# Kernel optimization log

Measured on AMD Instinct MI355X. Metric: run time of the kernel, lower is better.

## Reference

```python
import jax, jax.numpy as jnp
import numpy as np
from math import sqrt

B, T, C = 2, 2048, 2048
H = 16
NOPE, ROPE, VD, LORA = 128, 64, 128, 512
QK = NOPE + ROPE  # 192
EPS = 1e-6


def _make_freq_cis(T, rope_dim):
    inv = 1.0 / (10000.0 ** (np.arange(0, rope_dim, 2, dtype=np.float32) / rope_dim))
    t = np.arange(T, dtype=np.float32)
    ang = np.outer(t, inv)  # [T, rope_dim/2]
    return jnp.asarray(np.stack([np.cos(ang), np.sin(ang)], -1))  # [T, rope_dim/2, 2]


def setup_inputs() -> dict:
    key = jax.random.key(0)
    ks = jax.random.split(key, 6)
    x = jax.random.normal(ks[0], (B, T, C), jnp.float32)
    freq_cis = _make_freq_cis(T, ROPE)
    causal = jnp.where(jnp.tril(jnp.ones((T, T), bool)), 0.0, -1e9).astype(jnp.float32)
    Wq = jax.random.normal(ks[1], (C, H * QK), jnp.float32) * (1.0 / sqrt(C))
    Wckv = jax.random.normal(ks[2], (C, LORA + ROPE), jnp.float32) * (1.0 / sqrt(C))
    kv_norm_w = jnp.ones((LORA,), jnp.float32)
    Wdkv = jax.random.normal(ks[3], (LORA, H * (NOPE + VD)), jnp.float32) * (1.0 / sqrt(LORA))
    Wproj = jax.random.normal(ks[4], (H * VD, C), jnp.float32) * (1.0 / sqrt(H * VD))
    return {"x": x, "freq_cis": freq_cis, "mask": causal, "window": causal,
            "Wq": Wq, "Wckv": Wckv, "kv_norm_w": kv_norm_w, "Wdkv": Wdkv,
            "Wproj": Wproj, "start_pos": 0}


def apply_rope(x, freq_cis):
    # x: [B, T, h, D]; freq_cis: [T, D/2, 2]
    b, t, h, d = x.shape
    xr = x.reshape(b, t, h, d // 2, 2)
    fc = freq_cis.reshape(1, t, 1, d // 2, 2)
    real = xr[..., 0] * fc[..., 0] - xr[..., 1] * fc[..., 1]
    imag = xr[..., 1] * fc[..., 0] + xr[..., 0] * fc[..., 1]
    return jnp.stack([real, imag], -1).reshape(b, t, h, d)


def rms_norm(x, w, eps=EPS):
    return x * jax.lax.rsqrt(jnp.mean(x * x, -1, keepdims=True) + eps) * w


def reference(x, freq_cis, mask, window, Wq, Wckv, kv_norm_w, Wdkv, Wproj, start_pos):
    del window, start_pos  # Global attention, no KV cache (prefill)
    b, t, _ = x.shape
    q = (x @ Wq).reshape(b, t, H, QK)
    q_nope, q_rope = q[..., :NOPE], q[..., NOPE:]
    q_rope = apply_rope(q_rope, freq_cis)

    ckv = x @ Wckv  # [B, T, LORA+ROPE]
    kv_lat, k_rope = ckv[..., :LORA], ckv[..., LORA:]
    k_rope = apply_rope(k_rope.reshape(b, t, 1, ROPE), freq_cis)  # [B,T,1,ROPE]

    kv = rms_norm(kv_lat, kv_norm_w) @ Wdkv  # [B, T, H*(NOPE+VD)]
    kv = kv.reshape(b, t, H, NOPE + VD)
    k_nope, v = kv[..., :NOPE], kv[..., NOPE:]

    q = jnp.concatenate([q_nope, q_rope], -1)                                   # [B,T,H,QK]
    k = jnp.concatenate([k_nope, jnp.broadcast_to(k_rope, (b, t, H, ROPE))], -1)

    scale = 1.0 / sqrt(QK)
    atten = jnp.einsum('bqhd,bkhd->bhqk', q, k) * scale + mask  # [B,H,T,T]
    atten = jax.nn.softmax(atten, -1)
    out = jnp.einsum('bhqk,bkhd->bqhd', atten, v).reshape(b, t, H * VD)
    return out @ Wproj
```

## Files before the change

kernel.cpp:

```cpp
#include <hip/hip_runtime.h>
#include <hip/hip_bf16.h>
#include <math.h>


typedef short bf16x8 __attribute__((ext_vector_type(8)));
typedef short short4v __attribute__((ext_vector_type(4)));
typedef float f32x4 __attribute__((ext_vector_type(4)));
typedef float f32x16 __attribute__((ext_vector_type(16)));

#define MFMA16(a, b, c) __builtin_amdgcn_mfma_f32_16x16x32_bf16(a, b, c, 0, 0, 0)
#define MFMA32(a, b, c) __builtin_amdgcn_mfma_f32_32x32x16_bf16(a, b, c, 0, 0, 0)

__device__ __forceinline__ short f2bf(float f) {
  union { float f; unsigned u; } v; v.f = f;
  unsigned r = v.u + 0x7fffu + ((v.u >> 16) & 1u);
  return (short)(r >> 16);
}
__device__ __forceinline__ float bf2f(short s) {
  union { unsigned u; float f; } v;
  v.u = ((unsigned)(unsigned short)s) << 16;
  return v.f;
}
__device__ __forceinline__ unsigned cvtpk(float a, float b) {
  unsigned r;
  asm("v_cvt_pk_bf16_f32 %0, %1, %2" : "=v"(r) : "v"(a), "v"(b));
  return r;
}
__device__ __forceinline__ void gl16(const void* g, void* l) {
  __builtin_amdgcn_global_load_lds(
      (const __attribute__((address_space(1))) unsigned int*)g,
      (__attribute__((address_space(3))) unsigned int*)l, 16, 0, 0);
}
#define CFENCE() asm volatile("" ::: "memory")
#define HWBAR()  do { CFENCE(); __builtin_amdgcn_s_barrier(); CFENCE(); } while (0)

__global__ __launch_bounds__(256) void cvt_k(const float* __restrict__ in,
                                             short* __restrict__ out, int n) {
  int i = (blockIdx.x * 256 + threadIdx.x) * 8;
  if (i >= n) return;
  float4 a = *(const float4*)(in + i);
  float4 b = *(const float4*)(in + i + 4);
  bf16x8 o;
  o[0] = f2bf(a.x); o[1] = f2bf(a.y); o[2] = f2bf(a.z); o[3] = f2bf(a.w);
  o[4] = f2bf(b.x); o[5] = f2bf(b.y); o[6] = f2bf(b.z); o[7] = f2bf(b.w);
  *(bf16x8*)(out + i) = o;
}

__global__ __launch_bounds__(256) void tcvt_k(const float* __restrict__ W,
                                              short* __restrict__ out,
                                              int K, int N, int Np, int row_off) {
  __shared__ float tile[32][33];
  int k0 = blockIdx.x * 32, n0 = blockIdx.y * 32;
  int tx = threadIdx.x & 31, ty = threadIdx.x >> 5;
#pragma unroll
  for (int j = 0; j < 4; j++) {
    int k = k0 + ty + j * 8, n = n0 + tx;
    tile[ty + j * 8][tx] = (n < N) ? W[(size_t)k * N + n] : 0.f;
  }
  __syncthreads();
#pragma unroll
  for (int j = 0; j < 4; j++) {
    int n = n0 + ty + j * 8;
    out[(size_t)(row_off + n) * K + k0 + tx] = f2bf(tile[tx][ty + j * 8]);
  }
}

template <int MODE, int BM, int BN, int SGL>
__global__ __launch_bounds__(512, 2) void gemm8_k(const short* __restrict__ A,
                                                  const short* __restrict__ Bt,
                                                  void* __restrict__ C1,
                                                  void* __restrict__ C2,
                                                  int M, int N, int K, int nbx) {
  constexpr int FM = BM / 32;
  constexpr int FN = BN / 64;
  constexpr int XCH = (BM * 4) / 512;
  constexpr int YCH = (BN * 4) / 512;
  __shared__ short lX[3][BM * 32];
  __shared__ short lY[3][BN * 32];

  const int nwg = gridDim.x;
  const int cpx = nwg >> 3;
  const int swz = (blockIdx.x & 7) * cpx + (blockIdx.x >> 3);
  const int bx = swz % nbx, by = swz / nbx;
  const int m0 = bx * BM, n0 = by * BN;
  const int tid = threadIdx.x, lane = tid & 63, wave = tid >> 6;
  const int wm = wave >> 2, wn = wave & 3;
  const int l15 = lane & 15, l4 = lane >> 4;
  const int nt = K >> 5;

  auto stage = [&](int t) {
    int kk = t << 5;
    short* bX = &lX[t % 3][0];
    short* bY = &lY[t % 3][0];
#pragma unroll
    for (int c = 0; c < XCH; c++) {
      int idx = c * 512 + tid;
      int row = idx >> 2, seg = idx & 3;
      gl16(A + (size_t)(m0 + row) * K + kk + ((seg ^ ((row >> 1) & 3)) << 3),
           bX + idx * 8);
    }
#pragma unroll
    for (int c = 0; c < YCH; c++) {
      int idx = c * 512 + tid;
      int row = idx >> 2, seg = idx & 3;
      gl16(Bt + (size_t)(n0 + row) * K + kk + ((seg ^ ((row >> 1) & 3)) << 3),
           bY + idx * 8);
    }
  };

  f32x4 zero = {0.f, 0.f, 0.f, 0.f};
  f32x4 acc[FM][FN];
#pragma unroll
  for (int i = 0; i < FM; i++)
#pragma unroll
    for (int j = 0; j < FN; j++) acc[i][j] = zero;

  stage(0);
  stage(1);
  if constexpr (SGL == 4) asm volatile("s_waitcnt vmcnt(4)" ::: "memory");
  else                    asm volatile("s_waitcnt vmcnt(3)" ::: "memory");
  HWBAR();

  for (int t = 0; t < nt; t++) {
    const short* bX = &lX[t % 3][0];
    const short* bY = &lY[t % 3][0];
    bf16x8 xf[FM / 2], yf[FN];
#pragma unroll
    for (int i = 0; i < FM / 2; i++) {
      int row = wm * (BM / 2) + i * 16 + l15;
      xf[i] = *(const bf16x8*)&bX[row * 32 + ((l4 ^ ((row >> 1) & 3)) << 3)];
    }
#pragma unroll
    for (int j = 0; j < FN; j++) {
      int row = wn * (BN / 4) + j * 16 + l15;
      yf[j] = *(const bf16x8*)&bY[row * 32 + ((l4 ^ ((row >> 1) & 3)) << 3)];
    }
    bool st = (t + 2 < nt);
    if (st) stage(t + 2);
    HWBAR();
    __builtin_amdgcn_sched_barrier(0);
    __builtin_amdgcn_s_setprio(1);
#pragma unroll
    for (int i = 0; i < FM / 2; i++)
#pragma unroll
      for (int j = 0; j < FN; j++) acc[i][j] = MFMA16(xf[i], yf[j], acc[i][j]);
    __builtin_amdgcn_s_setprio(0);
    bf16x8 xg[FM / 2];
#pragma unroll
    for (int i = 0; i < FM / 2; i++) {
      int row = wm * (BM / 2) + (FM / 2 + i) * 16 + l15;
      xg[i] = *(const bf16x8*)&bX[row * 32 + ((l4 ^ ((row >> 1) & 3)) << 3)];
    }
    if (st) {
      if constexpr (SGL == 4) asm volatile("s_waitcnt vmcnt(4) lgkmcnt(0)" ::: "memory");
      else                    asm volatile("s_waitcnt vmcnt(3) lgkmcnt(0)" ::: "memory");
    } else {
      asm volatile("s_waitcnt vmcnt(0) lgkmcnt(0)" ::: "memory");
    }
    HWBAR();
    __builtin_amdgcn_sched_barrier(0);
    __builtin_amdgcn_s_setprio(1);
#pragma unroll
    for (int i = 0; i < FM / 2; i++)
#pragma unroll
      for (int j = 0; j < FN; j++)
        acc[FM / 2 + i][j] = MFMA16(xg[i], yf[j], acc[FM / 2 + i][j]);
    __builtin_amdgcn_s_setprio(0);
  }

#pragma unroll
  for (int i = 0; i < FM; i++) {
#pragma unroll
    for (int j = 0; j < FN; j++) {
      int m_ = m0 + wm * (BM / 2) + i * 16 + l4 * 4;
      int n = n0 + wn * (BN / 4) + j * 16 + l15;
      if (n >= N) continue;
      if (MODE == 2) {
        int bb = m_ >> 11, t2 = m_ & 2047, hh = n >> 8, c = n & 255;
        if (c < 128) {
#pragma unroll
          for (int r = 0; r < 4; r++)
            ((short*)C1)[((size_t)(bb * 16 + hh) * 2048 + t2 + r) * 192 + c] =
                f2bf(acc[i][j][r]);
        } else {
          short4v pk;
#pragma unroll
          for (int r = 0; r < 4; r++) pk[r] = f2bf(acc[i][j][r]);
          *(short4v*)&((short*)C2)[((size_t)(bb * 16 + hh) * 128 + (c - 128)) * 2048 + t2] = pk;
        }
      } else {
#pragma unroll
        for (int r = 0; r < 4; r++) {
          float v = acc[i][j][r];
          if (MODE == 0)
            ((short*)C1)[(size_t)(m_ + r) * N + n] = f2bf(v);
          else
            ((float*)C1)[(size_t)(m_ + r) * N + n] = v;
        }
      }
    }
  }
}

__global__ __launch_bounds__(256) void rmsnorm_k(const short* __restrict__ qc,
                                                 const float* __restrict__ w,
                                                 short* __restrict__ out) {
  int row = blockIdx.x * 4 + (threadIdx.x >> 6);
  int lane = threadIdx.x & 63;
  const short* src = qc + (size_t)row * 3712 + 3072 + lane * 8;
  bf16x8 v = *(const bf16x8*)src;
  float f[8];
  float ss = 0.f;
#pragma unroll
  for (int j = 0; j < 8; j++) { f[j] = bf2f(v[j]); ss += f[j] * f[j]; }
#pragma unroll
  for (int m = 1; m < 64; m <<= 1) ss += __shfl_xor(ss, m);
  float r = rsqrtf(ss * (1.f / 512.f) + 1e-6f);
  bf16x8 o;
#pragma unroll
  for (int j = 0; j < 8; j++) o[j] = f2bf(f[j] * r * w[lane * 8 + j]);
  *(bf16x8*)(out + (size_t)row * 512 + lane * 8) = o;
}

__global__ __launch_bounds__(256) void qrope_k(const short* __restrict__ qc,
                                               const float* __restrict__ freq,
                                               short* __restrict__ q_all) {
  int g = blockIdx.x * 256 + threadIdx.x;
  int row = g / 24, part = g % 24;
  int b = row >> 15, h = (row >> 11) & 15, t = row & 2047;
  const short* src = qc + (size_t)(b * 2048 + t) * 3712 + h * 192;
  short* dst = q_all + (size_t)row * 192;
  const float scale = 0.10411756f;
  if (part < 16) {
    bf16x8 v = *(const bf16x8*)(src + part * 8);
    bf16x8 o;
#pragma unroll
    for (int j = 0; j < 8; j++) o[j] = f2bf(bf2f(v[j]) * scale);
    *(bf16x8*)(dst + part * 8) = o;
  } else {
    int q = part - 16;
    bf16x8 v = *(const bf16x8*)(src + 128 + q * 8);
    float4 fa = *(const float4*)(freq + t * 64 + q * 8);
    float4 fb = *(const float4*)(freq + t * 64 + q * 8 + 4);
    float cs[8] = {fa.x, fa.y, fa.z, fa.w, fb.x, fb.y, fb.z, fb.w};
    bf16x8 o;
#pragma unroll
    for (int j = 0; j < 4; j++) {
      float c = cs[2 * j], s = cs[2 * j + 1];
      float x0 = bf2f(v[2 * j]), x1 = bf2f(v[2 * j + 1]);
      o[2 * j] = f2bf((x0 * c - x1 * s) * scale);
      o[2 * j + 1] = f2bf((x1 * c + x0 * s) * scale);
    }
    *(bf16x8*)(dst + 128 + q * 8) = o;
  }
}

__global__ __launch_bounds__(64) void krope_k(const short* __restrict__ qc,
                                              const float* __restrict__ freq,
                                              short* __restrict__ k_all) {
  int bt = blockIdx.x;
  int lane = threadIdx.x;
  int b = bt >> 11, t = bt & 2047;
  const short* src = qc + (size_t)bt * 3712 + 3584;
  int p = lane >> 1;
  float c = freq[t * 64 + p * 2], s = freq[t * 64 + p * 2 + 1];
  float x0 = bf2f(src[2 * p]), x1 = bf2f(src[2 * p + 1]);
  float v = (lane & 1) ? (x1 * c + x0 * s) : (x0 * c - x1 * s);
  short vb = f2bf(v);
#pragma unroll
  for (int h = 0; h < 16; h++)
    k_all[((size_t)(b * 16 + h) * 2048 + t) * 192 + 128 + lane] = vb;
}

__device__ __forceinline__ void stageK(const short* __restrict__ Kp,
                                       short* kb, int kt, int ptid) {
#pragma unroll
  for (int c = 0; c < 4; c++) {
    int idx = c * 256 + ptid;
    int r = idx / 25; if (r > 31) r = 31;
    int s = idx % 25;
    int s2 = (s >= 24) ? 0 : s;
    gl16(Kp + (size_t)(kt + r) * 192 + s2 * 8, kb + idx * 8);
  }
}

__global__ __launch_bounds__(512, 2) void attn_k(const short* __restrict__ q_all,
                                                 const short* __restrict__ k_all,
                                                 const short* __restrict__ vt,
                                                 short* __restrict__ attn_out) {
  __shared__ short kbuf[3][1024 * 8];
  int bh = blockIdx.x;
  int b = bh >> 4, h = bh & 15;
  int col = gridDim.y - 1 - blockIdx.y;
  int tid = threadIdx.x;
  int wave = tid >> 6, lane = tid & 63;
  int l31 = lane & 31, hi = lane >> 5;
  const bool producer = (wave >= 4);
  int qw = col * 128 + (wave & 3) * 32;
  int qrow = qw + l31;
  const short* Q = q_all + ((size_t)bh * 2048 + qrow) * 192;
  const short* Kp = k_all + (size_t)bh * 2048 * 192;
  const short* VT = vt + (size_t)bh * 128 * 2048;
  int sig = (l31 & 19) | ((l31 >> 1) & 4) | ((l31 << 1) & 8);

  bf16x8 qf[12];
  f32x16 o[4];
  f32x16 sInit, zro;
#pragma unroll
  for (int r = 0; r < 16; r++) { sInit[r] = -28.8539f; zro[r] = 0.f; }
  float lsum = 0.f;
  if (!producer) {
#pragma unroll
    for (int kb = 0; kb < 12; kb++)
      qf[kb] = *(const bf16x8*)(Q + kb * 16 + hi * 8);
#pragma unroll
    for (int vb = 0; vb < 4; vb++)
#pragma unroll
      for (int r = 0; r < 16; r++) o[vb][r] = 0.f;
  }

  const int nt = (col * 128 + 128) >> 5;

  if (producer) {
    stageK(Kp, kbuf[0], 0, tid - 256);
    if (nt > 1) stageK(Kp, kbuf[1], 32, tid - 256);
    asm volatile("s_waitcnt vmcnt(4)" ::: "memory");
  }
  HWBAR();

  for (int t = 0; t < nt; t++) {
    if (producer) {
      if (t + 2 < nt) {
        stageK(Kp, kbuf[(t + 2) % 3], (t + 2) << 5, tid - 256);
        asm volatile("s_waitcnt vmcnt(4)" ::: "memory");
      } else {
        asm volatile("s_waitcnt vmcnt(0)" ::: "memory");
      }
    } else {
      int kt = t << 5;
      int cur = t % 3;
      if (kt < qw + 32) {
        f32x16 sc = sInit, sc2 = zro;
        __builtin_amdgcn_s_setprio(1);
#pragma unroll
        for (int kb = 0; kb < 6; kb++) {
          int c0 = 2 * kb + hi, c1 = 2 * (kb + 6) + hi;
          bf16x8 kf0 = *(const bf16x8*)&kbuf[cur][sig * 200 + (c0 << 3)];
          bf16x8 kf1 = *(const bf16x8*)&kbuf[cur][sig * 200 + (c1 << 3)];
          sc = MFMA32(kf0, qf[kb], sc);
          sc2 = MFMA32(kf1, qf[kb + 6], sc2);
        }
        __builtin_amdgcn_s_setprio(0);
        bf16x8 v00 = *(const bf16x8*)(VT + (size_t)l31 * 2048 + kt + (hi << 3));
        bf16x8 v01 = *(const bf16x8*)(VT + (size_t)l31 * 2048 + kt + ((2 + hi) << 3));
        bf16x8 v10 = *(const bf16x8*)(VT + (size_t)(32 + l31) * 2048 + kt + (hi << 3));
        bf16x8 v11 = *(const bf16x8*)(VT + (size_t)(32 + l31) * 2048 + kt + ((2 + hi) << 3));
#pragma unroll
        for (int r = 0; r < 16; r++) sc[r] += sc2[r];
        unsigned pw[8];
        if (kt + 32 <= qw) {
#pragma unroll
          for (int r2 = 0; r2 < 8; r2++) {
            float pa = exp2f(sc[2 * r2]);
            float pb = exp2f(sc[2 * r2 + 1]);
            lsum += pa + pb;
            pw[r2] = cvtpk(pa, pb);
          }
        } else {
#pragma unroll
          for (int r2 = 0; r2 < 8; r2++) {
            int r = 2 * r2;
            int key = kt + (r & 3) + 4 * ((r >> 2) & 1) + 8 * hi + 16 * (r >> 3);
            float va = (key <= qrow) ? sc[r] : -1e30f;
            float vb2 = (key + 1 <= qrow) ? sc[r + 1] : -1e30f;
            float pa = exp2f(va);
            float pb = exp2f(vb2);
            lsum += pa + pb;
            pw[r2] = cvtpk(pa, pb);
          }
        }
        union { unsigned u[4]; bf16x8 v; } p0, p1;
#pragma unroll
        for (int w = 0; w < 4; w++) { p0.u[w] = pw[w]; p1.u[w] = pw[4 + w]; }
        bf16x8 v20 = *(const bf16x8*)(VT + (size_t)(64 + l31) * 2048 + kt + (hi << 3));
        bf16x8 v21 = *(const bf16x8*)(VT + (size_t)(64 + l31) * 2048 + kt + ((2 + hi) << 3));
        bf16x8 v30 = *(const bf16x8*)(VT + (size_t)(96 + l31) * 2048 + kt + (hi << 3));
        bf16x8 v31 = *(const bf16x8*)(VT + (size_t)(96 + l31) * 2048 + kt + ((2 + hi) << 3));
        __builtin_amdgcn_s_setprio(1);
        o[0] = MFMA32(v00, p0.v, o[0]); o[0] = MFMA32(v01, p1.v, o[0]);
        o[1] = MFMA32(v10, p0.v, o[1]); o[1] = MFMA32(v11, p1.v, o[1]);
        o[2] = MFMA32(v20, p0.v, o[2]); o[2] = MFMA32(v21, p1.v, o[2]);
        o[3] = MFMA32(v30, p0.v, o[3]); o[3] = MFMA32(v31, p1.v, o[3]);
        __builtin_amdgcn_s_setprio(0);
      }
    }
    HWBAR();
  }

  if (!producer) {
    lsum += __shfl_xor(lsum, 32);
    float inv = 1.f / lsum;
    size_t base = ((size_t)b * 2048 + qrow) * 2048 + h * 128;
#pragma unroll
    for (int vb = 0; vb < 4; vb++) {
#pragma unroll
      for (int r2 = 0; r2 < 8; r2++) {
        int r = 2 * r2;
        int v = vb * 32 + (r & 3) + 8 * (r >> 2) + 4 * hi;
        unsigned pk2 = ((unsigned)(unsigned short)f2bf(o[vb][r] * inv)) |
                       (((unsigned)(unsigned short)f2bf(o[vb][r + 1] * inv)) << 16);
        *(unsigned*)(attn_out + base + v) = pk2;
      }
    }
  }
}

extern "C" void kernel_launch(void* const* d_in, const int* in_sizes, int n_in,
                              void* d_out, int out_size, void* d_ws, size_t ws_size,
                              hipStream_t stream) {
  const float* x = (const float*)d_in[0];
  const float* freq = (const float*)d_in[1];
  const float* Wq = (const float*)d_in[4];
  const float* Wckv = (const float*)d_in[5];
  const float* kvw = (const float*)d_in[6];
  const float* Wdkv = (const float*)d_in[7];
  const float* Wproj = (const float*)d_in[8];

  char* ws = (char*)d_ws;
  size_t off = 0;
  auto alloc = [&](size_t bytes) {
    size_t o = off;
    off += (bytes + 255) & ~(size_t)255;
    return o;
  };
  size_t o_xbf = alloc(4096ull * 2048 * 2);
  size_t o_wqc = alloc(3840ull * 2048 * 2);
  size_t o_wdkv = alloc(4096ull * 512 * 2);
  size_t o_wproj = alloc(2048ull * 2048 * 2);
  size_t o_qc = alloc(4096ull * 3712 * 2);
  size_t o_kvlat = alloc(4096ull * 512 * 2);
  size_t o_qall = alloc(32ull * 2048 * 192 * 2);
  size_t o_kall = alloc(32ull * 2048 * 192 * 2);
  size_t o_vt = alloc(32ull * 128 * 2048 * 2);
  size_t o_attn = o_xbf;

  short* x_bf = (short*)(ws + o_xbf);
  short* wqc = (short*)(ws + o_wqc);
  short* wdkv = (short*)(ws + o_wdkv);
  short* wproj = (short*)(ws + o_wproj);
  short* qc = (short*)(ws + o_qc);
  short* kvlat = (short*)(ws + o_kvlat);
  short* qall = (short*)(ws + o_qall);
  short* kall = (short*)(ws + o_kall);
  short* vtb = (short*)(ws + o_vt);
  short* attnb = (short*)(ws + o_attn);

  cvt_k<<<4096, 256, 0, stream>>>(x, x_bf, 4096 * 2048);
  tcvt_k<<<dim3(64, 96), 256, 0, stream>>>(Wq, wqc, 2048, 3072, 3072, 0);
  tcvt_k<<<dim3(64, 24), 256, 0, stream>>>(Wckv, wqc, 2048, 576, 768, 3072);
  tcvt_k<<<dim3(16, 128), 256, 0, stream>>>(Wdkv, wdkv, 512, 4096, 4096, 0);
  tcvt_k<<<dim3(64, 64), 256, 0, stream>>>(Wproj, wproj, 2048, 2048, 2048, 0);

  gemm8_k<0, 256, 256, 4><<<240, 512, 0, stream>>>(x_bf, wqc, qc, nullptr,
                                                   4096, 3712, 2048, 16);

  rmsnorm_k<<<1024, 256, 0, stream>>>(qc, kvw, kvlat);
  qrope_k<<<6144, 256, 0, stream>>>(qc, freq, qall);
  krope_k<<<4096, 64, 0, stream>>>(qc, freq, kall);

  gemm8_k<2, 256, 256, 4><<<256, 512, 0, stream>>>(kvlat, wdkv, kall, vtb,
                                                   4096, 4096, 512, 16);

  attn_k<<<dim3(32, 16), 512, 0, stream>>>(qall, kall, vtb, attnb);

  gemm8_k<1, 128, 256, 3><<<256, 512, 0, stream>>>(attnb, wproj, d_out, nullptr,
                                                   4096, 2048, 2048, 32);
}
```

Measured before the change: 315.2 us.

## Stage V tiles through LDS via producer waves alongside K

Producer waves now stage V^T tiles into a triple-buffered shared-memory ring together with K, using async global-to-LDS copies. Consumer waves then read V fragments from LDS instead of issuing direct global loads in the PV loop. The aim is to take global-load latency off the consumer critical path and overlap it with compute. In exchange, LDS use per block grows, which may limit occupancy at two blocks per CU, and the padded row layout may cause bank conflicts.

```diff
diff --git a/kernel.cpp b/kernel.cpp
--- a/kernel.cpp
+++ b/kernel.cpp
@@ -272,15 +272,24 @@
     k_all[((size_t)(b * 16 + h) * 2048 + t) * 192 + 128 + lane] = vb;
 }
 
-__device__ __forceinline__ void stageK(const short* __restrict__ Kp,
-                                       short* kb, int kt, int ptid) {
-#pragma unroll
-  for (int c = 0; c < 4; c++) {
+__device__ __forceinline__ void stage6(const short* __restrict__ Kp,
+                                       const short* __restrict__ VT,
+                                       short* kb, short* vb, int kt, int ptid) {
+#pragma unroll
+  for (int c = 0; c < 6; c++) {
     int idx = c * 256 + ptid;
-    int r = idx / 25; if (r > 31) r = 31;
-    int s = idx % 25;
-    int s2 = (s >= 24) ? 0 : s;
-    gl16(Kp + (size_t)(kt + r) * 192 + s2 * 8, kb + idx * 8);
+    if (idx < 832) {
+      int r = idx / 25; if (r > 31) r = 31;
+      int s = idx % 25;
+      int s2 = (s >= 24) ? 0 : s;
+      gl16(Kp + (size_t)(kt + r) * 192 + s2 * 8, kb + idx * 8);
+    } else {
+      int v = idx - 832;
+      int r = v / 5; if (r > 127) r = 127;
+      int s = v % 5;
+      int s2 = (s >= 4) ? 0 : s;
+      gl16(VT + (size_t)r * 2048 + kt + s2 * 8, vb + v * 8);
+    }
   }
 }
 
@@ -288,7 +297,8 @@
                                                  const short* __restrict__ k_all,
                                                  const short* __restrict__ vt,
                                                  short* __restrict__ attn_out) {
-  __shared__ short kbuf[3][1024 * 8];
+  __shared__ short kbuf[3][832 * 8];
+  __shared__ short vbuf[3][704 * 8];
   int bh = blockIdx.x;
   int b = bh >> 4, h = bh & 15;
   int col = gridDim.y - 1 - blockIdx.y;
@@ -322,17 +332,17 @@
   const int nt = (col * 128 + 128) >> 5;
 
   if (producer) {
-    stageK(Kp, kbuf[0], 0, tid - 256);
-    if (nt > 1) stageK(Kp, kbuf[1], 32, tid - 256);
-    asm volatile("s_waitcnt vmcnt(4)" ::: "memory");
+    stage6(Kp, VT, kbuf[0], vbuf[0], 0, tid - 256);
+    if (nt > 1) stage6(Kp, VT, kbuf[1], vbuf[1], 32, tid - 256);
+    asm volatile("s_waitcnt vmcnt(6)" ::: "memory");
   }
   HWBAR();
 
   for (int t = 0; t < nt; t++) {
     if (producer) {
       if (t + 2 < nt) {
-        stageK(Kp, kbuf[(t + 2) % 3], (t + 2) << 5, tid - 256);
-        asm volatile("s_waitcnt vmcnt(4)" ::: "memory");
+        stage6(Kp, VT, kbuf[(t + 2) % 3], vbuf[(t + 2) % 3], (t + 2) << 5, tid - 256);
+        asm volatile("s_waitcnt vmcnt(6)" ::: "memory");
       } else {
         asm volatile("s_waitcnt vmcnt(0)" ::: "memory");
       }
@@ -351,10 +361,6 @@
           sc2 = MFMA32(kf1, qf[kb + 6], sc2);
         }
         __builtin_amdgcn_s_setprio(0);
-        bf16x8 v00 = *(const bf16x8*)(VT + (size_t)l31 * 2048 + kt + (hi << 3));
-        bf16x8 v01 = *(const bf16x8*)(VT + (size_t)l31 * 2048 + kt + ((2 + hi) << 3));
-        bf16x8 v10 = *(const bf16x8*)(VT + (size_t)(32 + l31) * 2048 + kt + (hi << 3));
-        bf16x8 v11 = *(const bf16x8*)(VT + (size_t)(32 + l31) * 2048 + kt + ((2 + hi) << 3));
 #pragma unroll
         for (int r = 0; r < 16; r++) sc[r] += sc2[r];
         unsigned pw[8];
@@ -382,15 +388,15 @@
         union { unsigned u[4]; bf16x8 v; } p0, p1;
 #pragma unroll
         for (int w = 0; w < 4; w++) { p0.u[w] = pw[w]; p1.u[w] = pw[4 + w]; }
-        bf16x8 v20 = *(const bf16x8*)(VT + (size_t)(64 + l31) * 2048 + kt + (hi << 3));
-        bf16x8 v21 = *(const bf16x8*)(VT + (size_t)(64 + l31) * 2048 + kt + ((2 + hi) << 3));
-        bf16x8 v30 = *(const bf16x8*)(VT + (size_t)(96 + l31) * 2048 + kt + (hi << 3));
-        bf16x8 v31 = *(const bf16x8*)(VT + (size_t)(96 + l31) * 2048 + kt + ((2 + hi) << 3));
         __builtin_amdgcn_s_setprio(1);
-        o[0] = MFMA32(v00, p0.v, o[0]); o[0] = MFMA32(v01, p1.v, o[0]);
-        o[1] = MFMA32(v10, p0.v, o[1]); o[1] = MFMA32(v11, p1.v, o[1]);
-        o[2] = MFMA32(v20, p0.v, o[2]); o[2] = MFMA32(v21, p1.v, o[2]);
-        o[3] = MFMA32(v30, p0.v, o[3]); o[3] = MFMA32(v31, p1.v, o[3]);
+#pragma unroll
+        for (int vb = 0; vb < 4; vb++) {
+          int vcol = vb * 32 + l31;
+          bf16x8 vf0 = *(const bf16x8*)&vbuf[cur][vcol * 40 + (hi << 3)];
+          bf16x8 vf1 = *(const bf16x8*)&vbuf[cur][vcol * 40 + ((2 + hi) << 3)];
+          o[vb] = MFMA32(vf0, p0.v, o[vb]);
+          o[vb] = MFMA32(vf1, p1.v, o[vb]);
+        }
         __builtin_amdgcn_s_setprio(0);
       }
     }
```

Result: faster. 275.0 us (-12.7%).
